# Kernel optimization log

Measured on AMD Instinct MI355X. Metric: run time of the kernel, lower is better.

The kernel has to match this reference:

```python
import jax, jax.numpy as jnp
import numpy as np

B, S, DIM_IN = 2, 2048, 1024
H, DQ, DK = 16, 64, 64


def setup_inputs() -> dict:
    key = jax.random.key(0)
    ks = jax.random.split(key, 11)
    s_in = 1.0 / np.sqrt(DIM_IN)
    s_o = 1.0 / np.sqrt(H * DK)
    return {
        "Q": jax.random.normal(ks[0], (B, S, DIM_IN), jnp.float32),
        "K": jax.random.normal(ks[1], (B, S, DIM_IN), jnp.float32),
        "V": jax.random.normal(ks[2], (B, S, DIM_IN), jnp.float32),
        # per-head projection weights, stacked over heads: [H, dim_in, d]
        "Wq": jax.random.uniform(ks[3], (H, DIM_IN, DQ), jnp.float32, -s_in, s_in),
        "bq": jax.random.uniform(ks[4], (H, DQ), jnp.float32, -s_in, s_in),
        "Wk": jax.random.uniform(ks[5], (H, DIM_IN, DK), jnp.float32, -s_in, s_in),
        "bk": jax.random.uniform(ks[6], (H, DK), jnp.float32, -s_in, s_in),
        "Wv": jax.random.uniform(ks[7], (H, DIM_IN, DK), jnp.float32, -s_in, s_in),
        "bv": jax.random.uniform(ks[8], (H, DK), jnp.float32, -s_in, s_in),
        # output projection: Linear(H*DK, DIM_IN)
        "Wo": jax.random.uniform(ks[9], (H * DK, DIM_IN), jnp.float32, -s_o, s_o),
        "bo": jax.random.uniform(ks[10], (DIM_IN,), jnp.float32, -s_o, s_o),
    }


def reference(Q, K, V, Wq, bq, Wk, bk, Wv, bv, Wo, bo):
    # per-head linear projections: [B,S,din] x [H,din,d] -> [B,H,S,d]
    q = jnp.einsum("bsd,hdq->bhsq", Q, Wq) + bq[None, :, None, :]
    k = jnp.einsum("bsd,hdk->bhsk", K, Wk) + bk[None, :, None, :]
    v = jnp.einsum("bsd,hdk->bhsk", V, Wv) + bv[None, :, None, :]
    # scaled dot-product attention (full NxN scores, as in the original)
    scores = jnp.einsum("bhsq,bhtq->bhst", q, k) / jnp.sqrt(jnp.asarray(DQ, q.dtype))
    attn = jax.nn.softmax(scores, axis=-1)
    o = jnp.einsum("bhst,bhtk->bhsk", attn, v)  # [B,H,S,DK]
    # concat heads along feature dim, then output projection
    o = o.transpose(0, 2, 1, 3).reshape(Q.shape[0], Q.shape[1], -1)  # [B,S,H*DK]
    return o @ Wo + bo
```

## Files before the change

kernel.cpp:

```cpp
#include <hip/hip_runtime.h>
#include <hip/hip_bf16.h>

#define DIN 1024
#define NH 16
#define HD 64
#define SEQ 2048
#define NB 2

typedef __attribute__((ext_vector_type(8))) short bf16x8;
typedef __attribute__((ext_vector_type(4))) float f32x4;
typedef __attribute__((ext_vector_type(16))) float f32x16;

__device__ inline short f2bf(float f) {
  union { float f; unsigned u; } v; v.f = f;
  unsigned r = v.u + 0x7fff + ((v.u >> 16) & 1);
  return (short)(r >> 16);
}

__device__ inline unsigned pk2(float lo, float hi) {
  unsigned r;
  asm("v_cvt_pk_bf16_f32 %0, %1, %2" : "=v"(r) : "v"(lo), "v"(hi));
  return r;
}

union U8 { unsigned u[4]; bf16x8 v; };
__device__ inline bf16x8 mkfrag(unsigned a, unsigned b, unsigned c, unsigned d) {
  U8 x; x.u[0] = a; x.u[1] = b; x.u[2] = c; x.u[3] = d; return x.v;
}

__device__ __forceinline__ void gload_lds16(const void* g, void* l) {
  __builtin_amdgcn_global_load_lds(
      (const __attribute__((address_space(1))) unsigned*)g,
      (__attribute__((address_space(3))) unsigned*)l, 16, 0, 0);
}

__global__ __launch_bounds__(256) void cvt_kernel(
    const float* __restrict__ Q, const float* __restrict__ K, const float* __restrict__ V,
    short* __restrict__ xq, short* __restrict__ xk, short* __restrict__ xv) {
  int z = blockIdx.y;
  const float* src = z == 0 ? Q : (z == 1 ? K : V);
  short* dst = z == 0 ? xq : (z == 1 ? xk : xv);
  size_t e = ((size_t)blockIdx.x * 256 + threadIdx.x) * 8;
  float4 x0 = *(const float4*)(src + e);
  float4 x1 = *(const float4*)(src + e + 4);
  bf16x8 v;
  v[0] = f2bf(x0.x); v[1] = f2bf(x0.y); v[2] = f2bf(x0.z); v[3] = f2bf(x0.w);
  v[4] = f2bf(x1.x); v[5] = f2bf(x1.y); v[6] = f2bf(x1.z); v[7] = f2bf(x1.w);
  *(bf16x8*)(dst + e) = v;
}

__global__ __launch_bounds__(256) void wt3_kernel(
    const float* __restrict__ Wq, const float* __restrict__ Wk, const float* __restrict__ Wv,
    short* __restrict__ out) {
  int zz = blockIdx.z; int which = zz >> 4, h = zz & 15;
  const float* in = (which == 0 ? Wq : (which == 1 ? Wk : Wv)) + (size_t)h * (DIN * HD);
  short* o = out + (size_t)which * (NH * HD * DIN) + (size_t)h * (HD * DIN);
  __shared__ float tile[64][65];
  int r0 = blockIdx.y * 64;
  int t = threadIdx.x;
  int r = t >> 2, cc = (t & 3) * 16;
#pragma unroll
  for (int j = 0; j < 16; ++j) tile[r][cc + j] = in[(size_t)(r0 + r) * HD + cc + j];
  __syncthreads();
  int c = t >> 2, rr = (t & 3) * 16;
#pragma unroll
  for (int j = 0; j < 16; ++j) o[(size_t)c * DIN + r0 + rr + j] = f2bf(tile[rr + j][c]);
}

__global__ __launch_bounds__(256) void wt_kernel(const float* __restrict__ in,
                                                 short* __restrict__ out, int R, int C) {
  __shared__ float tile[64][65];
  int r0 = blockIdx.y * 64, c0 = blockIdx.x * 64;
  int t = threadIdx.x;
  int r = t >> 2, cc = (t & 3) * 16;
#pragma unroll
  for (int j = 0; j < 16; ++j) tile[r][cc + j] = in[(size_t)(r0 + r) * C + c0 + cc + j];
  __syncthreads();
  int c = t >> 2, rr = (t & 3) * 16;
#pragma unroll
  for (int j = 0; j < 16; ++j) out[(size_t)(c0 + c) * R + r0 + rr + j] = f2bf(tile[rr + j][c]);
}

#define QSCL 0.18033688011112042f

__global__ __launch_bounds__(256) void proj_bf16_kernel(
    const short* __restrict__ xq, const short* __restrict__ xk, const short* __restrict__ xv,
    const short* __restrict__ wt,
    const float* __restrict__ bq, const float* __restrict__ bk, const float* __restrict__ bv,
    short* __restrict__ qb, short* __restrict__ kb, short* __restrict__ vt) {
  int mt = blockIdx.x, nt = blockIdx.y, z = blockIdx.z;
  const short* A = z == 0 ? xq : (z == 1 ? xk : xv);
  const short* Bt = wt + (size_t)z * (DIN * DIN);
  const float* bias = z == 0 ? bq : (z == 1 ? bk : bv);

  __shared__ __align__(16) short Al[128 * 32];
  __shared__ __align__(16) short Bl[128 * 32];

  int t = threadIdx.x, wid = t >> 6, lane = t & 63;
  int lrow = lane & 15, lhi = lane >> 4;
  int wr = wid >> 1, wc = wid & 1;
  int row0 = mt * 128, col0 = nt * 128;

  const short* aG = A + (size_t)(row0 + wid * 16 + (lane >> 2)) * DIN + (lane & 3) * 8;
  const short* bG = Bt + (size_t)(col0 + wid * 16 + (lane >> 2)) * DIN + (lane & 3) * 8;
  short* aL0 = &Al[wid * 512];
  short* aL1 = &Al[(4 + wid) * 512];
  short* bL0 = &Bl[wid * 512];
  short* bL1 = &Bl[(4 + wid) * 512];
  const short* aR = &Al[(wr * 64 + lrow) * 32 + lhi * 8];
  const short* bR = &Bl[(wc * 64 + lrow) * 32 + lhi * 8];

  f32x4 acc[4][4] = {};
  for (int kk = 0; kk < DIN; kk += 32) {
    gload_lds16(aG + kk, aL0);
    gload_lds16(aG + 64 * DIN + kk, aL1);
    gload_lds16(bG + kk, bL0);
    gload_lds16(bG + 64 * DIN + kk, bL1);
    __syncthreads();
    bf16x8 af[4], bfv[4];
#pragma unroll
    for (int m = 0; m < 4; ++m) af[m] = *(const bf16x8*)(aR + m * 512);
#pragma unroll
    for (int n = 0; n < 4; ++n) bfv[n] = *(const bf16x8*)(bR + n * 512);
#pragma unroll
    for (int m = 0; m < 4; ++m)
#pragma unroll
      for (int n = 0; n < 4; ++n)
        acc[m][n] = __builtin_amdgcn_mfma_f32_16x16x32_bf16(af[m], bfv[n], acc[m][n], 0, 0, 0);
    __syncthreads();
  }

#pragma unroll
  for (int m = 0; m < 4; ++m) {
#pragma unroll
    for (int n = 0; n < 4; ++n) {
      int c = col0 + wc * 64 + n * 16 + lrow;
      int h = c >> 6, hc = c & 63;
      float bval = bias[c];
#pragma unroll
      for (int i = 0; i < 4; ++i) {
        int r = row0 + wr * 64 + m * 16 + lhi * 4 + i;
        int b = r >> 11, s = r & 2047;
        float val = acc[m][n][i] + bval;
        if (z == 0) val *= QSCL;
        if (z == 2) vt[((size_t)(b * NH + h) * HD + hc) * SEQ + s] = f2bf(val);
        else {
          short* o = z == 0 ? qb : kb;
          o[((size_t)(b * NH + h) * SEQ + s) * HD + hc] = f2bf(val);
        }
      }
    }
  }
}

__global__ __launch_bounds__(256) void proj_f32_kernel(
    const float* __restrict__ Q, const float* __restrict__ K, const float* __restrict__ V,
    const short* __restrict__ wt,
    const float* __restrict__ bq, const float* __restrict__ bk, const float* __restrict__ bv,
    short* __restrict__ qb, short* __restrict__ kb, short* __restrict__ vt) {
  int mt = blockIdx.x, nt = blockIdx.y, z = blockIdx.z;
  const float* X = z == 0 ? Q : (z == 1 ? K : V);
  const short* Bt = wt + (size_t)z * (DIN * DIN);
  const float* bias = z == 0 ? bq : (z == 1 ? bk : bv);

  __shared__ __align__(16) short Al[128 * 32];
  __shared__ __align__(16) short Bl[128 * 32];

  int t = threadIdx.x, wid = t >> 6, lane = t & 63;
  int lrow = lane & 15, lhi = lane >> 4;
  int wr = wid >> 1, wc = wid & 1;
  int row0 = mt * 128, col0 = nt * 128;

  int arow = t >> 1, acol = (t & 1) * 16;
  const float* aF = X + (size_t)(row0 + arow) * DIN + acol;
  short* aW = &Al[arow * 32 + acol];

  const short* bG = Bt + (size_t)(col0 + wid * 16 + (lane >> 2)) * DIN + (lane & 3) * 8;
  short* bL0 = &Bl[wid * 512];
  short* bL1 = &Bl[(4 + wid) * 512];

  const short* aR = &Al[(wr * 64 + lrow) * 32 + lhi * 8];
  const short* bR = &Bl[(wc * 64 + lrow) * 32 + lhi * 8];

  f32x4 acc[4][4] = {};
  for (int kk = 0; kk < DIN; kk += 32) {
    gload_lds16(bG + kk, bL0);
    gload_lds16(bG + 64 * DIN + kk, bL1);
    float4 x0 = *(const float4*)(aF + kk);
    float4 x1 = *(const float4*)(aF + kk + 4);
    float4 x2 = *(const float4*)(aF + kk + 8);
    float4 x3 = *(const float4*)(aF + kk + 12);
    bf16x8 v0, v1;
    v0[0] = f2bf(x0.x); v0[1] = f2bf(x0.y); v0[2] = f2bf(x0.z); v0[3] = f2bf(x0.w);
    v0[4] = f2bf(x1.x); v0[5] = f2bf(x1.y); v0[6] = f2bf(x1.z); v0[7] = f2bf(x1.w);
    v1[0] = f2bf(x2.x); v1[1] = f2bf(x2.y); v1[2] = f2bf(x2.z); v1[3] = f2bf(x2.w);
    v1[4] = f2bf(x3.x); v1[5] = f2bf(x3.y); v1[6] = f2bf(x3.z); v1[7] = f2bf(x3.w);
    *(bf16x8*)aW = v0;
    *(bf16x8*)(aW + 8) = v1;
    __syncthreads();
    bf16x8 af[4], bfv[4];
#pragma unroll
    for (int m = 0; m < 4; ++m) af[m] = *(const bf16x8*)(aR + m * 512);
#pragma unroll
    for (int n = 0; n < 4; ++n) bfv[n] = *(const bf16x8*)(bR + n * 512);
#pragma unroll
    for (int m = 0; m < 4; ++m)
#pragma unroll
      for (int n = 0; n < 4; ++n)
        acc[m][n] = __builtin_amdgcn_mfma_f32_16x16x32_bf16(af[m], bfv[n], acc[m][n], 0, 0, 0);
    __syncthreads();
  }
#pragma unroll
  for (int m = 0; m < 4; ++m) {
#pragma unroll
    for (int n = 0; n < 4; ++n) {
      int c = col0 + wc * 64 + n * 16 + lrow;
      int h = c >> 6, hc = c & 63;
      float bval = bias[c];
#pragma unroll
      for (int i = 0; i < 4; ++i) {
        int r = row0 + wr * 64 + m * 16 + lhi * 4 + i;
        int b = r >> 11, s = r & 2047;
        float val = acc[m][n][i] + bval;
        if (z == 0) val *= QSCL;
        if (z == 2) vt[((size_t)(b * NH + h) * HD + hc) * SEQ + s] = f2bf(val);
        else {
          short* o = z == 0 ? qb : kb;
          o[((size_t)(b * NH + h) * SEQ + s) * HD + hc] = f2bf(val);
        }
      }
    }
  }
}

__global__ __launch_bounds__(256) void attn_kernel(
    const short* __restrict__ qb, const short* __restrict__ kb,
    const short* __restrict__ vt, short* __restrict__ ob) {
  int qt = blockIdx.x, h = blockIdx.y, bz = blockIdx.z;
  int t = threadIdx.x, wid = t >> 6, lane = t & 63;
  int l31 = lane & 31, hi = lane >> 5;

  __shared__ __align__(16) short kl[2][64 * 64];
  __shared__ __align__(16) short vl[2][64 * 64];

  size_t bh = (size_t)(bz * NH + h);
  const short* kbase = kb + bh * (size_t)SEQ * HD;
  const short* vbase = vt + bh * (size_t)HD * SEQ;

  int qg = qt * 128 + wid * 32 + l31;
  const short* qrow = qb + (bh * SEQ + qg) * HD + hi * 8;
  bf16x8 qf0 = *(const bf16x8*)(qrow);
  bf16x8 qf1 = *(const bf16x8*)(qrow + 16);
  bf16x8 qf2 = *(const bf16x8*)(qrow + 32);
  bf16x8 qf3 = *(const bf16x8*)(qrow + 48);

  int srow = wid * 16 + (lane >> 3);
  int swc = ((lane & 7) ^ (srow & 7)) * 8;
  const short* kg = kbase + (size_t)srow * HD + swc;
  const short* vg = vbase + (size_t)srow * SEQ + swc;

  f32x16 o0, o1;
#pragma unroll
  for (int i = 0; i < 16; ++i) { o0[i] = 0.f; o1[i] = 0.f; }
  float mrun = -1e30f, lrun = 0.f;

  int ksw = (l31 & 7) << 3;

#define STAGE(T0, B)                                                   \
  do {                                                                 \
    gload_lds16(kg + (size_t)(T0)*HD, &kl[B][wid * 1024]);             \
    gload_lds16(kg + (size_t)((T0) + 8) * HD, &kl[B][wid * 1024 + 512]); \
    gload_lds16(vg + (T0), &vl[B][wid * 1024]);                        \
    gload_lds16(vg + (T0) + 8 * SEQ, &vl[B][wid * 1024 + 512]);        \
  } while (0)

  STAGE(0, 0);
  __syncthreads();
  int cur = 0;

  for (int t0 = 0; t0 < SEQ; t0 += 64) {
    if (t0 + 64 < SEQ) STAGE(t0 + 64, cur ^ 1);

    f32x16 c0, c1;
#pragma unroll
    for (int i = 0; i < 16; ++i) { c0[i] = 0.f; c1[i] = 0.f; }
#pragma unroll
    for (int dk = 0; dk < 4; ++dk) {
      int col = (dk * 16 + hi * 8) ^ ksw;
      bf16x8 ka = *(const bf16x8*)&kl[cur][l31 * 64 + col];
      bf16x8 kc = *(const bf16x8*)&kl[cur][(32 + l31) * 64 + col];
      bf16x8 qv = dk == 0 ? qf0 : dk == 1 ? qf1 : dk == 2 ? qf2 : qf3;
      c0 = __builtin_amdgcn_mfma_f32_32x32x16_bf16(ka, qv, c0, 0, 0, 0);
      c1 = __builtin_amdgcn_mfma_f32_32x32x16_bf16(kc, qv, c1, 0, 0, 0);
    }

    float tm[16];
#pragma unroll
    for (int i = 0; i < 16; ++i) tm[i] = fmaxf(c0[i], c1[i]);
#pragma unroll
    for (int i = 0; i < 8; ++i) tm[i] = fmaxf(tm[i], tm[i + 8]);
#pragma unroll
    for (int i = 0; i < 4; ++i) tm[i] = fmaxf(tm[i], tm[i + 4]);
    float mx = fmaxf(fmaxf(tm[0], tm[1]), fmaxf(tm[2], tm[3]));
    mx = fmaxf(mx, __shfl_xor(mx, 32));
    if (!__all(mx - mrun <= 8.f)) {
      float mnew = fmaxf(mrun, mx);
      float corr = __builtin_amdgcn_exp2f(mrun - mnew);
      lrun *= corr;
#pragma unroll
      for (int i = 0; i < 16; ++i) { o0[i] *= corr; o1[i] *= corr; }
      mrun = mnew;
    }
#pragma unroll
    for (int i = 0; i < 16; ++i) c0[i] = __builtin_amdgcn_exp2f(c0[i] - mrun);
#pragma unroll
    for (int i = 0; i < 16; ++i) c1[i] = __builtin_amdgcn_exp2f(c1[i] - mrun);
    float ts[16];
#pragma unroll
    for (int i = 0; i < 16; ++i) ts[i] = c0[i] + c1[i];
#pragma unroll
    for (int i = 0; i < 8; ++i) ts[i] += ts[i + 8];
#pragma unroll
    for (int i = 0; i < 4; ++i) ts[i] += ts[i + 4];
    float ps = (ts[0] + ts[1]) + (ts[2] + ts[3]);
    ps += __shfl_xor(ps, 32);
    lrun += ps;

    unsigned u0 = pk2(c0[0], c0[1]),   u1 = pk2(c0[2], c0[3]);
    unsigned u2 = pk2(c0[4], c0[5]),   u3 = pk2(c0[6], c0[7]);
    unsigned u4 = pk2(c0[8], c0[9]),   u5 = pk2(c0[10], c0[11]);
    unsigned u6 = pk2(c0[12], c0[13]), u7 = pk2(c0[14], c0[15]);
    unsigned w0 = pk2(c1[0], c1[1]),   w1 = pk2(c1[2], c1[3]);
    unsigned w2 = pk2(c1[4], c1[5]),   w3 = pk2(c1[6], c1[7]);
    unsigned w4 = pk2(c1[8], c1[9]),   w5 = pk2(c1[10], c1[11]);
    unsigned w6 = pk2(c1[12], c1[13]), w7 = pk2(c1[14], c1[15]);
    unsigned x0 = __shfl_xor(u0, 32), x1 = __shfl_xor(u1, 32);
    unsigned x2 = __shfl_xor(u2, 32), x3 = __shfl_xor(u3, 32);
    unsigned x4 = __shfl_xor(u4, 32), x5 = __shfl_xor(u5, 32);
    unsigned x6 = __shfl_xor(u6, 32), x7 = __shfl_xor(u7, 32);
    unsigned y0 = __shfl_xor(w0, 32), y1 = __shfl_xor(w1, 32);
    unsigned y2 = __shfl_xor(w2, 32), y3 = __shfl_xor(w3, 32);
    unsigned y4 = __shfl_xor(w4, 32), y5 = __shfl_xor(w5, 32);
    unsigned y6 = __shfl_xor(w6, 32), y7 = __shfl_xor(w7, 32);
    bf16x8 fA0 = mkfrag(hi ? x2 : u0, hi ? x3 : u1, hi ? u2 : x0, hi ? u3 : x1);
    bf16x8 fA1 = mkfrag(hi ? x6 : u4, hi ? x7 : u5, hi ? u6 : x4, hi ? u7 : x5);
    bf16x8 fB0 = mkfrag(hi ? y2 : w0, hi ? y3 : w1, hi ? w2 : y0, hi ? w3 : y1);
    bf16x8 fB1 = mkfrag(hi ? y6 : w4, hi ? y7 : w5, hi ? w6 : y4, hi ? w7 : y5);

#pragma unroll
    for (int kc4 = 0; kc4 < 4; ++kc4) {
      bf16x8 pf = kc4 == 0 ? fA0 : kc4 == 1 ? fA1 : kc4 == 2 ? fB0 : fB1;
      int col = (kc4 * 16 + hi * 8) ^ ksw;
      bf16x8 va = *(const bf16x8*)&vl[cur][l31 * 64 + col];
      bf16x8 vb = *(const bf16x8*)&vl[cur][(32 + l31) * 64 + col];
      o0 = __builtin_amdgcn_mfma_f32_32x32x16_bf16(va, pf, o0, 0, 0, 0);
      o1 = __builtin_amdgcn_mfma_f32_32x32x16_bf16(vb, pf, o1, 0, 0, 0);
    }
    __syncthreads();
    cur ^= 1;
  }
#undef STAGE

  float inv = 1.0f / lrun;
  short* orow = ob + ((size_t)(bz * SEQ + qg)) * DIN + h * HD;
#pragma unroll
  for (int r = 0; r < 16; ++r) {
    int d = (r & 3) + 8 * (r >> 2) + 4 * hi;
    orow[d] = f2bf(o0[r] * inv);
    orow[32 + d] = f2bf(o1[r] * inv);
  }
}

__global__ __launch_bounds__(256) void oproj_kernel(
    const short* __restrict__ ob, const short* __restrict__ wto,
    const float* __restrict__ bo, float* __restrict__ out) {
  int mt = blockIdx.x, nt = blockIdx.y;
  __shared__ __align__(16) short Al[64 * 32];
  __shared__ __align__(16) short Bl[128 * 32];
  int t = threadIdx.x, wid = t >> 6, lane = t & 63;
  int lrow = lane & 15, lhi = lane >> 4;
  int wr = wid >> 1, wc = wid & 1;
  int row0 = mt * 64, col0 = nt * 128;

  const short* aG = ob + (size_t)(row0 + wid * 16 + (lane >> 2)) * DIN + (lane & 3) * 8;
  const short* bG = wto + (size_t)(col0 + wid * 16 + (lane >> 2)) * DIN + (lane & 3) * 8;
  short* aL = &Al[wid * 512];
  short* bL0 = &Bl[wid * 512];
  short* bL1 = &Bl[(4 + wid) * 512];
  const short* aR = &Al[(wr * 32 + lrow) * 32 + lhi * 8];
  const short* bR = &Bl[(wc * 64 + lrow) * 32 + lhi * 8];

  f32x4 acc[2][4] = {};
  for (int kk = 0; kk < DIN; kk += 32) {
    gload_lds16(aG + kk, aL);
    gload_lds16(bG + kk, bL0);
    gload_lds16(bG + 64 * DIN + kk, bL1);
    __syncthreads();
    bf16x8 af[2], bfv[4];
#pragma unroll
    for (int m = 0; m < 2; ++m) af[m] = *(const bf16x8*)(aR + m * 512);
#pragma unroll
    for (int n = 0; n < 4; ++n) bfv[n] = *(const bf16x8*)(bR + n * 512);
#pragma unroll
    for (int m = 0; m < 2; ++m)
#pragma unroll
      for (int n = 0; n < 4; ++n)
        acc[m][n] = __builtin_amdgcn_mfma_f32_16x16x32_bf16(af[m], bfv[n], acc[m][n], 0, 0, 0);
    __syncthreads();
  }
#pragma unroll
  for (int m = 0; m < 2; ++m) {
#pragma unroll
    for (int n = 0; n < 4; ++n) {
      int c = col0 + wc * 64 + n * 16 + lrow;
      float bval = bo[c];
#pragma unroll
      for (int i = 0; i < 4; ++i) {
        int r = row0 + wr * 32 + m * 16 + lhi * 4 + i;
        out[(size_t)r * DIN + c] = acc[m][n][i] + bval;
      }
    }
  }
}

extern "C" void kernel_launch(void* const* d_in, const int* in_sizes, int n_in,
                              void* d_out, int out_size, void* d_ws, size_t ws_size,
                              hipStream_t stream) {
  const float* Q  = (const float*)d_in[0];
  const float* K  = (const float*)d_in[1];
  const float* V  = (const float*)d_in[2];
  const float* Wq = (const float*)d_in[3];
  const float* bq = (const float*)d_in[4];
  const float* Wk = (const float*)d_in[5];
  const float* bk = (const float*)d_in[6];
  const float* Wv = (const float*)d_in[7];
  const float* bv = (const float*)d_in[8];
  const float* Wo = (const float*)d_in[9];
  const float* bo = (const float*)d_in[10];
  float* out = (float*)d_out;

  short* ws = (short*)d_ws;
  const size_t NX = (size_t)NB * SEQ * DIN;
  const size_t NW = (size_t)NH * HD * DIN;
  short* qbuf = ws;
  short* kbuf = qbuf + NX;
  short* vtb  = kbuf + NX;
  short* obuf = vtb + NX;
  short* wtq  = obuf + NX;
  short* wto  = wtq + 3 * NW;
  short* xq = wto + NW;
  short* xk = xq + NX;
  short* xv = xk + NX;
  const size_t need_big = (7 * NX + 4 * NW) * sizeof(short);

  wt3_kernel<<<dim3(1, 16, 48), 256, 0, stream>>>(Wq, Wk, Wv, wtq);
  wt_kernel<<<dim3(16, 16, 1), 256, 0, stream>>>(Wo, wto, DIN, DIN);
  if (ws_size >= need_big) {
    cvt_kernel<<<dim3(2048, 3), 256, 0, stream>>>(Q, K, V, xq, xk, xv);
    proj_bf16_kernel<<<dim3(32, 8, 3), 256, 0, stream>>>(xq, xk, xv, wtq, bq, bk, bv,
                                                         qbuf, kbuf, vtb);
  } else {
    proj_f32_kernel<<<dim3(32, 8, 3), 256, 0, stream>>>(Q, K, V, wtq, bq, bk, bv,
                                                        qbuf, kbuf, vtb);
  }
  attn_kernel<<<dim3(16, 16, 2), 256, 0, stream>>>(qbuf, kbuf, vtb, obuf);
  oproj_kernel<<<dim3(64, 8), 256, 0, stream>>>(obuf, wto, bo, out);
}
```

Baseline: 245.4 us.

## Widen attention KV tile to 128, use permlane32 swap, fuse fp32 cast into projection

The attention kernel now processes 128 keys per iteration: it stages two 64-key K/V sub-tiles per buffer and computes four score blocks per step, so it runs half as many online-softmax rescales and barriers. The cross-half P fragment exchange now uses v_permlane32_swap in place of shfl_xor plus selects. The separate fp32-to-bf16 conversion kernel is removed and the projection reads fp32 inputs directly, converting them with packed bf16 instructions. In exchange, the attention kernel doubles its LDS use and carries more live registers, which may lower occupancy.

```diff
diff --git a/kernel.cpp b/kernel.cpp
--- a/kernel.cpp
+++ b/kernel.cpp
@@ -10,6 +10,7 @@
 typedef __attribute__((ext_vector_type(8))) short bf16x8;
 typedef __attribute__((ext_vector_type(4))) float f32x4;
 typedef __attribute__((ext_vector_type(16))) float f32x16;
+typedef __attribute__((ext_vector_type(4))) unsigned u32x4;
 
 __device__ inline short f2bf(float f) {
   union { float f; unsigned u; } v; v.f = f;
@@ -23,6 +24,10 @@
   return r;
 }
 
+__device__ inline void pl32swap(unsigned& a, unsigned& b) {
+  asm("v_permlane32_swap_b32 %0, %1" : "+v"(a), "+v"(b));
+}
+
 union U8 { unsigned u[4]; bf16x8 v; };
 __device__ inline bf16x8 mkfrag(unsigned a, unsigned b, unsigned c, unsigned d) {
   U8 x; x.u[0] = a; x.u[1] = b; x.u[2] = c; x.u[3] = d; return x.v;
@@ -32,21 +37,6 @@
   __builtin_amdgcn_global_load_lds(
       (const __attribute__((address_space(1))) unsigned*)g,
       (__attribute__((address_space(3))) unsigned*)l, 16, 0, 0);
-}
-
-__global__ __launch_bounds__(256) void cvt_kernel(
-    const float* __restrict__ Q, const float* __restrict__ K, const float* __restrict__ V,
-    short* __restrict__ xq, short* __restrict__ xk, short* __restrict__ xv) {
-  int z = blockIdx.y;
-  const float* src = z == 0 ? Q : (z == 1 ? K : V);
-  short* dst = z == 0 ? xq : (z == 1 ? xk : xv);
-  size_t e = ((size_t)blockIdx.x * 256 + threadIdx.x) * 8;
-  float4 x0 = *(const float4*)(src + e);
-  float4 x1 = *(const float4*)(src + e + 4);
-  bf16x8 v;
-  v[0] = f2bf(x0.x); v[1] = f2bf(x0.y); v[2] = f2bf(x0.z); v[3] = f2bf(x0.w);
-  v[4] = f2bf(x1.x); v[5] = f2bf(x1.y); v[6] = f2bf(x1.z); v[7] = f2bf(x1.w);
-  *(bf16x8*)(dst + e) = v;
 }
 
 __global__ __launch_bounds__(256) void wt3_kernel(
@@ -83,13 +73,13 @@
 
 #define QSCL 0.18033688011112042f
 
-__global__ __launch_bounds__(256) void proj_bf16_kernel(
-    const short* __restrict__ xq, const short* __restrict__ xk, const short* __restrict__ xv,
+__global__ __launch_bounds__(256) void proj_kernel(
+    const float* __restrict__ Q, const float* __restrict__ K, const float* __restrict__ V,
     const short* __restrict__ wt,
     const float* __restrict__ bq, const float* __restrict__ bk, const float* __restrict__ bv,
     short* __restrict__ qb, short* __restrict__ kb, short* __restrict__ vt) {
   int mt = blockIdx.x, nt = blockIdx.y, z = blockIdx.z;
-  const short* A = z == 0 ? xq : (z == 1 ? xk : xv);
+  const float* X = z == 0 ? Q : (z == 1 ? K : V);
   const short* Bt = wt + (size_t)z * (DIN * DIN);
   const float* bias = z == 0 ? bq : (z == 1 ? bk : bv);
 
@@ -101,21 +91,32 @@
   int wr = wid >> 1, wc = wid & 1;
   int row0 = mt * 128, col0 = nt * 128;
 
-  const short* aG = A + (size_t)(row0 + wid * 16 + (lane >> 2)) * DIN + (lane & 3) * 8;
+  int arow = t >> 1, acol = (t & 1) * 16;
+  const float* aF = X + (size_t)(row0 + arow) * DIN + acol;
+  short* aW = &Al[arow * 32 + acol];
+
   const short* bG = Bt + (size_t)(col0 + wid * 16 + (lane >> 2)) * DIN + (lane & 3) * 8;
-  short* aL0 = &Al[wid * 512];
-  short* aL1 = &Al[(4 + wid) * 512];
   short* bL0 = &Bl[wid * 512];
   short* bL1 = &Bl[(4 + wid) * 512];
+
   const short* aR = &Al[(wr * 64 + lrow) * 32 + lhi * 8];
   const short* bR = &Bl[(wc * 64 + lrow) * 32 + lhi * 8];
 
   f32x4 acc[4][4] = {};
   for (int kk = 0; kk < DIN; kk += 32) {
-    gload_lds16(aG + kk, aL0);
-    gload_lds16(aG + 64 * DIN + kk, aL1);
     gload_lds16(bG + kk, bL0);
     gload_lds16(bG + 64 * DIN + kk, bL1);
+    float4 x0 = *(const float4*)(aF + kk);
+    float4 x1 = *(const float4*)(aF + kk + 4);
+    float4 x2 = *(const float4*)(aF + kk + 8);
+    float4 x3 = *(const float4*)(aF + kk + 12);
+    u32x4 pA, pB;
+    pA[0] = pk2(x0.x, x0.y); pA[1] = pk2(x0.z, x0.w);
+    pA[2] = pk2(x1.x, x1.y); pA[3] = pk2(x1.z, x1.w);
+    pB[0] = pk2(x2.x, x2.y); pB[1] = pk2(x2.z, x2.w);
+    pB[2] = pk2(x3.x, x3.y); pB[3] = pk2(x3.z, x3.w);
+    *(u32x4*)aW = pA;
+    *(u32x4*)(aW + 8) = pB;
     __syncthreads();
     bf16x8 af[4], bfv[4];
 #pragma unroll
@@ -129,7 +130,6 @@
         acc[m][n] = __builtin_amdgcn_mfma_f32_16x16x32_bf16(af[m], bfv[n], acc[m][n], 0, 0, 0);
     __syncthreads();
   }
-
 #pragma unroll
   for (int m = 0; m < 4; ++m) {
 #pragma unroll
@@ -153,86 +153,6 @@
   }
 }
 
-__global__ __launch_bounds__(256) void proj_f32_kernel(
-    const float* __restrict__ Q, const float* __restrict__ K, const float* __restrict__ V,
-    const short* __restrict__ wt,
-    const float* __restrict__ bq, const float* __restrict__ bk, const float* __restrict__ bv,
-    short* __restrict__ qb, short* __restrict__ kb, short* __restrict__ vt) {
-  int mt = blockIdx.x, nt = blockIdx.y, z = blockIdx.z;
-  const float* X = z == 0 ? Q : (z == 1 ? K : V);
-  const short* Bt = wt + (size_t)z * (DIN * DIN);
-  const float* bias = z == 0 ? bq : (z == 1 ? bk : bv);
-
-  __shared__ __align__(16) short Al[128 * 32];
-  __shared__ __align__(16) short Bl[128 * 32];
-
-  int t = threadIdx.x, wid = t >> 6, lane = t & 63;
-  int lrow = lane & 15, lhi = lane >> 4;
-  int wr = wid >> 1, wc = wid & 1;
-  int row0 = mt * 128, col0 = nt * 128;
-
-  int arow = t >> 1, acol = (t & 1) * 16;
-  const float* aF = X + (size_t)(row0 + arow) * DIN + acol;
-  short* aW = &Al[arow * 32 + acol];
-
-  const short* bG = Bt + (size_t)(col0 + wid * 16 + (lane >> 2)) * DIN + (lane & 3) * 8;
-  short* bL0 = &Bl[wid * 512];
-  short* bL1 = &Bl[(4 + wid) * 512];
-
-  const short* aR = &Al[(wr * 64 + lrow) * 32 + lhi * 8];
-  const short* bR = &Bl[(wc * 64 + lrow) * 32 + lhi * 8];
-
-  f32x4 acc[4][4] = {};
-  for (int kk = 0; kk < DIN; kk += 32) {
-    gload_lds16(bG + kk, bL0);
-    gload_lds16(bG + 64 * DIN + kk, bL1);
-    float4 x0 = *(const float4*)(aF + kk);
-    float4 x1 = *(const float4*)(aF + kk + 4);
-    float4 x2 = *(const float4*)(aF + kk + 8);
-    float4 x3 = *(const float4*)(aF + kk + 12);
-    bf16x8 v0, v1;
-    v0[0] = f2bf(x0.x); v0[1] = f2bf(x0.y); v0[2] = f2bf(x0.z); v0[3] = f2bf(x0.w);
-    v0[4] = f2bf(x1.x); v0[5] = f2bf(x1.y); v0[6] = f2bf(x1.z); v0[7] = f2bf(x1.w);
-    v1[0] = f2bf(x2.x); v1[1] = f2bf(x2.y); v1[2] = f2bf(x2.z); v1[3] = f2bf(x2.w);
-    v1[4] = f2bf(x3.x); v1[5] = f2bf(x3.y); v1[6] = f2bf(x3.z); v1[7] = f2bf(x3.w);
-    *(bf16x8*)aW = v0;
-    *(bf16x8*)(aW + 8) = v1;
-    __syncthreads();
-    bf16x8 af[4], bfv[4];
-#pragma unroll
-    for (int m = 0; m < 4; ++m) af[m] = *(const bf16x8*)(aR + m * 512);
-#pragma unroll
-    for (int n = 0; n < 4; ++n) bfv[n] = *(const bf16x8*)(bR + n * 512);
-#pragma unroll
-    for (int m = 0; m < 4; ++m)
-#pragma unroll
-      for (int n = 0; n < 4; ++n)
-        acc[m][n] = __builtin_amdgcn_mfma_f32_16x16x32_bf16(af[m], bfv[n], acc[m][n], 0, 0, 0);
-    __syncthreads();
-  }
-#pragma unroll
-  for (int m = 0; m < 4; ++m) {
-#pragma unroll
-    for (int n = 0; n < 4; ++n) {
-      int c = col0 + wc * 64 + n * 16 + lrow;
-      int h = c >> 6, hc = c & 63;
-      float bval = bias[c];
-#pragma unroll
-      for (int i = 0; i < 4; ++i) {
-        int r = row0 + wr * 64 + m * 16 + lhi * 4 + i;
-        int b = r >> 11, s = r & 2047;
-        float val = acc[m][n][i] + bval;
-        if (z == 0) val *= QSCL;
-        if (z == 2) vt[((size_t)(b * NH + h) * HD + hc) * SEQ + s] = f2bf(val);
-        else {
-          short* o = z == 0 ? qb : kb;
-          o[((size_t)(b * NH + h) * SEQ + s) * HD + hc] = f2bf(val);
-        }
-      }
-    }
-  }
-}
-
 __global__ __launch_bounds__(256) void attn_kernel(
     const short* __restrict__ qb, const short* __restrict__ kb,
     const short* __restrict__ vt, short* __restrict__ ob) {
@@ -240,8 +160,8 @@
   int t = threadIdx.x, wid = t >> 6, lane = t & 63;
   int l31 = lane & 31, hi = lane >> 5;
 
-  __shared__ __align__(16) short kl[2][64 * 64];
-  __shared__ __align__(16) short vl[2][64 * 64];
+  __shared__ __align__(16) short kl[2][2][64 * 64];
+  __shared__ __align__(16) short vl[2][2][64 * 64];
 
   size_t bh = (size_t)(bz * NH + h);
   const short* kbase = kb + bh * (size_t)SEQ * HD;
@@ -266,37 +186,45 @@
 
   int ksw = (l31 & 7) << 3;
 
-#define STAGE(T0, B)                                                   \
-  do {                                                                 \
-    gload_lds16(kg + (size_t)(T0)*HD, &kl[B][wid * 1024]);             \
-    gload_lds16(kg + (size_t)((T0) + 8) * HD, &kl[B][wid * 1024 + 512]); \
-    gload_lds16(vg + (T0), &vl[B][wid * 1024]);                        \
-    gload_lds16(vg + (T0) + 8 * SEQ, &vl[B][wid * 1024 + 512]);        \
+#define STAGE(T0, B)                                                        \
+  do {                                                                      \
+    gload_lds16(kg + (size_t)(T0)*HD, &kl[B][0][wid * 1024]);               \
+    gload_lds16(kg + (size_t)((T0) + 8) * HD, &kl[B][0][wid * 1024 + 512]); \
+    gload_lds16(kg + (size_t)((T0) + 64) * HD, &kl[B][1][wid * 1024]);      \
+    gload_lds16(kg + (size_t)((T0) + 72) * HD, &kl[B][1][wid * 1024 + 512]);\
+    gload_lds16(vg + (T0), &vl[B][0][wid * 1024]);                          \
+    gload_lds16(vg + (T0) + 8 * SEQ, &vl[B][0][wid * 1024 + 512]);          \
+    gload_lds16(vg + (T0) + 64, &vl[B][1][wid * 1024]);                     \
+    gload_lds16(vg + (T0) + 64 + 8 * SEQ, &vl[B][1][wid * 1024 + 512]);     \
   } while (0)
 
   STAGE(0, 0);
   __syncthreads();
   int cur = 0;
 
-  for (int t0 = 0; t0 < SEQ; t0 += 64) {
-    if (t0 + 64 < SEQ) STAGE(t0 + 64, cur ^ 1);
-
-    f32x16 c0, c1;
-#pragma unroll
-    for (int i = 0; i < 16; ++i) { c0[i] = 0.f; c1[i] = 0.f; }
+  for (int t0 = 0; t0 < SEQ; t0 += 128) {
+    if (t0 + 128 < SEQ) STAGE(t0 + 128, cur ^ 1);
+
+    f32x16 cA0, cA1, cB0, cB1;
+#pragma unroll
+    for (int i = 0; i < 16; ++i) { cA0[i] = 0.f; cA1[i] = 0.f; cB0[i] = 0.f; cB1[i] = 0.f; }
 #pragma unroll
     for (int dk = 0; dk < 4; ++dk) {
       int col = (dk * 16 + hi * 8) ^ ksw;
-      bf16x8 ka = *(const bf16x8*)&kl[cur][l31 * 64 + col];
-      bf16x8 kc = *(const bf16x8*)&kl[cur][(32 + l31) * 64 + col];
       bf16x8 qv = dk == 0 ? qf0 : dk == 1 ? qf1 : dk == 2 ? qf2 : qf3;
-      c0 = __builtin_amdgcn_mfma_f32_32x32x16_bf16(ka, qv, c0, 0, 0, 0);
-      c1 = __builtin_amdgcn_mfma_f32_32x32x16_bf16(kc, qv, c1, 0, 0, 0);
+      bf16x8 kA0 = *(const bf16x8*)&kl[cur][0][l31 * 64 + col];
+      bf16x8 kA1 = *(const bf16x8*)&kl[cur][0][(32 + l31) * 64 + col];
+      bf16x8 kB0 = *(const bf16x8*)&kl[cur][1][l31 * 64 + col];
+      bf16x8 kB1 = *(const bf16x8*)&kl[cur][1][(32 + l31) * 64 + col];
+      cA0 = __builtin_amdgcn_mfma_f32_32x32x16_bf16(kA0, qv, cA0, 0, 0, 0);
+      cA1 = __builtin_amdgcn_mfma_f32_32x32x16_bf16(kA1, qv, cA1, 0, 0, 0);
+      cB0 = __builtin_amdgcn_mfma_f32_32x32x16_bf16(kB0, qv, cB0, 0, 0, 0);
+      cB1 = __builtin_amdgcn_mfma_f32_32x32x16_bf16(kB1, qv, cB1, 0, 0, 0);
     }
 
     float tm[16];
 #pragma unroll
-    for (int i = 0; i < 16; ++i) tm[i] = fmaxf(c0[i], c1[i]);
+    for (int i = 0; i < 16; ++i) tm[i] = fmaxf(fmaxf(cA0[i], cA1[i]), fmaxf(cB0[i], cB1[i]));
 #pragma unroll
     for (int i = 0; i < 8; ++i) tm[i] = fmaxf(tm[i], tm[i + 8]);
 #pragma unroll
@@ -312,12 +240,16 @@
       mrun = mnew;
     }
 #pragma unroll
-    for (int i = 0; i < 16; ++i) c0[i] = __builtin_amdgcn_exp2f(c0[i] - mrun);
-#pragma unroll
-    for (int i = 0; i < 16; ++i) c1[i] = __builtin_amdgcn_exp2f(c1[i] - mrun);
+    for (int i = 0; i < 16; ++i) cA0[i] = __builtin_amdgcn_exp2f(cA0[i] - mrun);
+#pragma unroll
+    for (int i = 0; i < 16; ++i) cA1[i] = __builtin_amdgcn_exp2f(cA1[i] - mrun);
+#pragma unroll
+    for (int i = 0; i < 16; ++i) cB0[i] = __builtin_amdgcn_exp2f(cB0[i] - mrun);
+#pragma unroll
+    for (int i = 0; i < 16; ++i) cB1[i] = __builtin_amdgcn_exp2f(cB1[i] - mrun);
     float ts[16];
 #pragma unroll
-    for (int i = 0; i < 16; ++i) ts[i] = c0[i] + c1[i];
+    for (int i = 0; i < 16; ++i) ts[i] = (cA0[i] + cA1[i]) + (cB0[i] + cB1[i]);
 #pragma unroll
     for (int i = 0; i < 8; ++i) ts[i] += ts[i + 8];
 #pragma unroll
@@ -326,33 +258,50 @@
     ps += __shfl_xor(ps, 32);
     lrun += ps;
 
-    unsigned u0 = pk2(c0[0], c0[1]),   u1 = pk2(c0[2], c0[3]);
-    unsigned u2 = pk2(c0[4], c0[5]),   u3 = pk2(c0[6], c0[7]);
-    unsigned u4 = pk2(c0[8], c0[9]),   u5 = pk2(c0[10], c0[11]);
-    unsigned u6 = pk2(c0[12], c0[13]), u7 = pk2(c0[14], c0[15]);
-    unsigned w0 = pk2(c1[0], c1[1]),   w1 = pk2(c1[2], c1[3]);
-    unsigned w2 = pk2(c1[4], c1[5]),   w3 = pk2(c1[6], c1[7]);
-    unsigned w4 = pk2(c1[8], c1[9]),   w5 = pk2(c1[10], c1[11]);
-    unsigned w6 = pk2(c1[12], c1[13]), w7 = pk2(c1[14], c1[15]);
-    unsigned x0 = __shfl_xor(u0, 32), x1 = __shfl_xor(u1, 32);
-    unsigned x2 = __shfl_xor(u2, 32), x3 = __shfl_xor(u3, 32);
-    unsigned x4 = __shfl_xor(u4, 32), x5 = __shfl_xor(u5, 32);
-    unsigned x6 = __shfl_xor(u6, 32), x7 = __shfl_xor(u7, 32);
-    unsigned y0 = __shfl_xor(w0, 32), y1 = __shfl_xor(w1, 32);
-    unsigned y2 = __shfl_xor(w2, 32), y3 = __shfl_xor(w3, 32);
-    unsigned y4 = __shfl_xor(w4, 32), y5 = __shfl_xor(w5, 32);
-    unsigned y6 = __shfl_xor(w6, 32), y7 = __shfl_xor(w7, 32);
-    bf16x8 fA0 = mkfrag(hi ? x2 : u0, hi ? x3 : u1, hi ? u2 : x0, hi ? u3 : x1);
-    bf16x8 fA1 = mkfrag(hi ? x6 : u4, hi ? x7 : u5, hi ? u6 : x4, hi ? u7 : x5);
-    bf16x8 fB0 = mkfrag(hi ? y2 : w0, hi ? y3 : w1, hi ? w2 : y0, hi ? w3 : y1);
-    bf16x8 fB1 = mkfrag(hi ? y6 : w4, hi ? y7 : w5, hi ? w6 : y4, hi ? w7 : y5);
+    unsigned u0 = pk2(cA0[0], cA0[1]),   u1 = pk2(cA0[2], cA0[3]);
+    unsigned u2 = pk2(cA0[4], cA0[5]),   u3 = pk2(cA0[6], cA0[7]);
+    unsigned u4 = pk2(cA0[8], cA0[9]),   u5 = pk2(cA0[10], cA0[11]);
+    unsigned u6 = pk2(cA0[12], cA0[13]), u7 = pk2(cA0[14], cA0[15]);
+    pl32swap(u0, u2); pl32swap(u1, u3); pl32swap(u4, u6); pl32swap(u5, u7);
+    bf16x8 fA0 = mkfrag(u0, u1, u2, u3);
+    bf16x8 fA1 = mkfrag(u4, u5, u6, u7);
+    unsigned v0 = pk2(cA1[0], cA1[1]),   v1 = pk2(cA1[2], cA1[3]);
+    unsigned v2 = pk2(cA1[4], cA1[5]),   v3 = pk2(cA1[6], cA1[7]);
+    unsigned v4 = pk2(cA1[8], cA1[9]),   v5 = pk2(cA1[10], cA1[11]);
+    unsigned v6 = pk2(cA1[12], cA1[13]), v7 = pk2(cA1[14], cA1[15]);
+    pl32swap(v0, v2); pl32swap(v1, v3); pl32swap(v4, v6); pl32swap(v5, v7);
+    bf16x8 fA2 = mkfrag(v0, v1, v2, v3);
+    bf16x8 fA3 = mkfrag(v4, v5, v6, v7);
+    unsigned w0 = pk2(cB0[0], cB0[1]),   w1 = pk2(cB0[2], cB0[3]);
+    unsigned w2 = pk2(cB0[4], cB0[5]),   w3 = pk2(cB0[6], cB0[7]);
+    unsigned w4 = pk2(cB0[8], cB0[9]),   w5 = pk2(cB0[10], cB0[11]);
+    unsigned w6 = pk2(cB0[12], cB0[13]), w7 = pk2(cB0[14], cB0[15]);
+    pl32swap(w0, w2); pl32swap(w1, w3); pl32swap(w4, w6); pl32swap(w5, w7);
+    bf16x8 fB0 = mkfrag(w0, w1, w2, w3);
+    bf16x8 fB1 = mkfrag(w4, w5, w6, w7);
+    unsigned y0 = pk2(cB1[0], cB1[1]),   y1 = pk2(cB1[2], cB1[3]);
+    unsigned y2 = pk2(cB1[4], cB1[5]),   y3 = pk2(cB1[6], cB1[7]);
+    unsigned y4 = pk2(cB1[8], cB1[9]),   y5 = pk2(cB1[10], cB1[11]);
+    unsigned y6 = pk2(cB1[12], cB1[13]), y7 = pk2(cB1[14], cB1[15]);
+    pl32swap(y0, y2); pl32swap(y1, y3); pl32swap(y4, y6); pl32swap(y5, y7);
+    bf16x8 fB2 = mkfrag(y0, y1, y2, y3);
+    bf16x8 fB3 = mkfrag(y4, y5, y6, y7);
 
 #pragma unroll
     for (int kc4 = 0; kc4 < 4; ++kc4) {
-      bf16x8 pf = kc4 == 0 ? fA0 : kc4 == 1 ? fA1 : kc4 == 2 ? fB0 : fB1;
+      bf16x8 pf = kc4 == 0 ? fA0 : kc4 == 1 ? fA1 : kc4 == 2 ? fA2 : fA3;
       int col = (kc4 * 16 + hi * 8) ^ ksw;
-      bf16x8 va = *(const bf16x8*)&vl[cur][l31 * 64 + col];
-      bf16x8 vb = *(const bf16x8*)&vl[cur][(32 + l31) * 64 + col];
+      bf16x8 va = *(const bf16x8*)&vl[cur][0][l31 * 64 + col];
+      bf16x8 vb = *(const bf16x8*)&vl[cur][0][(32 + l31) * 64 + col];
+      o0 = __builtin_amdgcn_mfma_f32_32x32x16_bf16(va, pf, o0, 0, 0, 0);
+      o1 = __builtin_amdgcn_mfma_f32_32x32x16_bf16(vb, pf, o1, 0, 0, 0);
+    }
+#pragma unroll
+    for (int kc4 = 0; kc4 < 4; ++kc4) {
+      bf16x8 pf = kc4 == 0 ? fB0 : kc4 == 1 ? fB1 : kc4 == 2 ? fB2 : fB3;
+      int col = (kc4 * 16 + hi * 8) ^ ksw;
+      bf16x8 va = *(const bf16x8*)&vl[cur][1][l31 * 64 + col];
+      bf16x8 vb = *(const bf16x8*)&vl[cur][1][(32 + l31) * 64 + col];
       o0 = __builtin_amdgcn_mfma_f32_32x32x16_bf16(va, pf, o0, 0, 0, 0);
       o1 = __builtin_amdgcn_mfma_f32_32x32x16_bf16(vb, pf, o1, 0, 0, 0);
     }
@@ -448,21 +397,11 @@
   short* obuf = vtb + NX;
   short* wtq  = obuf + NX;
   short* wto  = wtq + 3 * NW;
-  short* xq = wto + NW;
-  short* xk = xq + NX;
-  short* xv = xk + NX;
-  const size_t need_big = (7 * NX + 4 * NW) * sizeof(short);
 
   wt3_kernel<<<dim3(1, 16, 48), 256, 0, stream>>>(Wq, Wk, Wv, wtq);
   wt_kernel<<<dim3(16, 16, 1), 256, 0, stream>>>(Wo, wto, DIN, DIN);
-  if (ws_size >= need_big) {
-    cvt_kernel<<<dim3(2048, 3), 256, 0, stream>>>(Q, K, V, xq, xk, xv);
-    proj_bf16_kernel<<<dim3(32, 8, 3), 256, 0, stream>>>(xq, xk, xv, wtq, bq, bk, bv,
-                                                         qbuf, kbuf, vtb);
-  } else {
-    proj_f32_kernel<<<dim3(32, 8, 3), 256, 0, stream>>>(Q, K, V, wtq, bq, bk, bv,
-                                                        qbuf, kbuf, vtb);
-  }
+  proj_kernel<<<dim3(32, 8, 3), 256, 0, stream>>>(Q, K, V, wtq, bq, bk, bv,
+                                                  qbuf, kbuf, vtb);
   attn_kernel<<<dim3(16, 16, 2), 256, 0, stream>>>(qbuf, kbuf, vtb, obuf);
   oproj_kernel<<<dim3(64, 8), 256, 0, stream>>>(obuf, wto, bo, out);
 }
```

After: 254.5 us. +3.7%, slower.
